# Kernel tuning notes

Hardware: AMD Instinct MI355X
Metric: run time of the kernel (lower is better)

Reference implementation:

```python
import jax, jax.numpy as jnp
import numpy as np

B, L = 64, 8192
WIN = 3            # unfold window size
H = 90             # surrogate MLP hidden width (brains-py default)
N_ELEC = 7         # total electrodes; data on 2,3,4; controls on 0,1,5,6
AMP = 28.5         # electrode_effects amplification


def setup_inputs() -> dict:
    key = jax.random.key(0)
    ks = jax.random.split(key, 16)
    x = jax.random.normal(ks[0], (B, L), dtype=jnp.float32)
    # 4 learned control voltages (electrodes 0,1,5,6), plausible voltage range
    cv = jax.random.uniform(ks[1], (4,), dtype=jnp.float32, minval=-1.2, maxval=0.6)
    def lin(k, fan_in, fan_out):
        w = jax.random.normal(k, (fan_in, fan_out), dtype=jnp.float32) * np.sqrt(2.0 / fan_in).astype(np.float32)
        return w
    W1 = lin(ks[2], N_ELEC, H); b1 = jnp.zeros((H,), jnp.float32)
    W2 = lin(ks[3], H, H);      b2 = jnp.zeros((H,), jnp.float32)
    W3 = lin(ks[4], H, H);      b3 = jnp.zeros((H,), jnp.float32)
    W4 = lin(ks[5], H, H);      b4 = jnp.zeros((H,), jnp.float32)
    W5 = lin(ks[6], H, H);      b5 = jnp.zeros((H,), jnp.float32)
    W6 = lin(ks[7], H, 1);      b6 = jnp.zeros((1,), jnp.float32)
    return {"x": x, "cv": cv,
            "W1": W1, "b1": b1, "W2": W2, "b2": b2, "W3": W3, "b3": b3,
            "W4": W4, "b4": b4, "W5": W5, "b5": b5, "W6": W6, "b6": b6}


def reference(x, cv, W1, b1, W2, b2, W3, b3, W4, b4, W5, b5, W6, b6):
    Bq, Lq = x.shape
    n_win = Lq - WIN + 1
    # sliding windows (unfold(1, 3, 1)): [B, n_win, 3]
    idx = jnp.arange(n_win)[:, None] + jnp.arange(WIN)[None, :]
    win = x[:, idx]  # [B, n_win, 3]
    # assemble 7-electrode input: cv[0:2] | data window | cv[2:4]
    cv_lo = jnp.broadcast_to(cv[:2], (Bq, n_win, 2))
    cv_hi = jnp.broadcast_to(cv[2:], (Bq, n_win, 2))
    z = jnp.concatenate([cv_lo, win, cv_hi], axis=-1)  # [B, n_win, 7]
    h = jax.nn.relu(z @ W1 + b1)
    h = jax.nn.relu(h @ W2 + b2)
    h = jax.nn.relu(h @ W3 + b3)
    h = jax.nn.relu(h @ W4 + b4)
    h = jax.nn.relu(h @ W5 + b5)
    out = (h @ W6 + b6) * AMP  # [B, n_win, 1]
    return out[..., 0]  # squeeze -> [B, n_win]
```

## Files before the change

### kernel.cpp

```cpp
#include <hip/hip_runtime.h>

#define NB   64
#define LSEQ 8192
#define NW   8190
#define HD   90
#define AMPF 28.5f
#define NTILE 2

typedef _Float16 half8  __attribute__((ext_vector_type(8)));
typedef float    f32x16 __attribute__((ext_vector_type(16)));
typedef __fp16   fp16x2 __attribute__((ext_vector_type(2)));

union FragU { uint4 u; half8 h; };

__device__ __forceinline__ unsigned pk2(float a, float b) {
  fp16x2 v = __builtin_amdgcn_cvt_pkrtz(a, b);
  return __builtin_bit_cast(unsigned, v);
}
__device__ __forceinline__ unsigned pkmax0(unsigned w) {
  unsigned r;
  asm("v_pk_max_f16 %0, %1, %2" : "=v"(r) : "v"(w), "v"(0u));
  return r;
}

__global__ void dnpu_pack(const float* __restrict__ W1, const float* __restrict__ b1,
                          const float* __restrict__ W2, const float* __restrict__ b2,
                          const float* __restrict__ W3, const float* __restrict__ b3,
                          const float* __restrict__ W4, const float* __restrict__ b4,
                          const float* __restrict__ W5, const float* __restrict__ b5,
                          const float* __restrict__ W6, const float* __restrict__ b6,
                          uint4* __restrict__ frags) {
  int tid = blockIdx.x * blockDim.x + threadIdx.x;
  if (tid >= 81 * 64) return;
  int f = tid >> 6, lane = tid & 63;
  int n = lane & 31, g = lane >> 5;
  const float* W; const float* bias; int t2, ks, kin, nout;
  if (f < 3) {
    W = W1; bias = b1; t2 = f; ks = 0; kin = 7; nout = HD;
  } else if (f < 75) {
    int q = f - 3; int L = q / 18; int r = q % 18;
    t2 = r / 6; ks = r % 6; kin = HD; nout = HD;
    W    = (L == 0) ? W2 : (L == 1) ? W3 : (L == 2) ? W4 : W5;
    bias = (L == 0) ? b2 : (L == 1) ? b3 : (L == 2) ? b4 : b5;
  } else {
    W = W6; bias = b6; t2 = 0; ks = f - 75; kin = HD; nout = 1;
  }
  int row = 32 * t2 + n;
  FragU u;
#pragma unroll
  for (int i = 0; i < 8; ++i) {
    int k = 16 * ks + 8 * g + i;
    float val = 0.f;
    if (row < nout) {
      if (k < kin)       val = W[k * nout + row];
      else if (k == kin) val = bias[row];
    }
    if (row == HD && k == kin && f < 75) val = 1.0f;
    u.h[i] = (_Float16)val;
  }
  frags[f * 64 + lane] = u.u;
}

__device__ __forceinline__ void trans_u(const f32x16& a, uint4& b0, uint4& b1) {
  unsigned p00 = pkmax0(pk2(a[0],  a[1]));
  unsigned p10 = pkmax0(pk2(a[2],  a[3]));
  unsigned p01 = pkmax0(pk2(a[4],  a[5]));
  unsigned p11 = pkmax0(pk2(a[6],  a[7]));
  unsigned p02 = pkmax0(pk2(a[8],  a[9]));
  unsigned p12 = pkmax0(pk2(a[10], a[11]));
  unsigned p03 = pkmax0(pk2(a[12], a[13]));
  unsigned p13 = pkmax0(pk2(a[14], a[15]));
  asm("v_permlane32_swap_b32 %0, %1" : "+v"(p00), "+v"(p01));
  asm("v_permlane32_swap_b32 %0, %1" : "+v"(p10), "+v"(p11));
  b0 = make_uint4(p00, p10, p01, p11);
  asm("v_permlane32_swap_b32 %0, %1" : "+v"(p02), "+v"(p03));
  asm("v_permlane32_swap_b32 %0, %1" : "+v"(p12), "+v"(p13));
  b1 = make_uint4(p02, p12, p03, p13);
}

__device__ __forceinline__ void hidden_layer_t(const uint4* __restrict__ src, int lane,
                                               uint4 (&B)[6]) {
  uint4 Bn[6];
#pragma unroll
  for (int u = 0; u < 3; ++u) {
    f32x16 a = (f32x16)(0.f);
#pragma unroll
    for (int ks = 0; ks < 6; ++ks) {
      FragU Af; Af.u = src[(u * 6 + ks) * 64 + lane];
      a = __builtin_amdgcn_mfma_f32_32x32x16_f16(
            Af.h, __builtin_bit_cast(half8, B[ks]), a, 0, 0, 0);
    }
    trans_u(a, Bn[2 * u], Bn[2 * u + 1]);
  }
#pragma unroll
  for (int i = 0; i < 6; ++i) B[i] = Bn[i];
}

__global__ __launch_bounds__(512, 2)
void dnpu_mfma(const float* __restrict__ x, const float* __restrict__ cv,
               const uint4* __restrict__ frags, float* __restrict__ out) {
  __shared__ uint4 lfr[72 * 64];
  const int tid  = threadIdx.x;
  const int lane = tid & 63, wid = tid >> 6;
  const int g = lane >> 5, c = lane & 31;
  const int b = blockIdx.y;

  for (int i = tid; i < 72 * 64; i += 512) lfr[i] = frags[3 * 64 + i];
  __syncthreads();

  const float c0 = cv[0], c1 = cv[1], c2 = cv[2], c3 = cv[3];
  const float* xr = x + (size_t)b * LSEQ;
  const int rowbase0 = blockIdx.x * (NTILE * 32 * 8) + wid * (NTILE * 32);

  uint4 Bw[NTILE][6];

#pragma unroll
  for (int t = 0; t < NTILE; ++t) {
    const int w  = rowbase0 + t * 32 + c;
    const int xi = (w < LSEQ - 3) ? w : (LSEQ - 3);
    const float x0 = xr[xi], x1 = xr[xi + 1], x2 = xr[xi + 2];
    half8 B1;
#pragma unroll
    for (int i = 0; i < 8; ++i) B1[i] = (_Float16)0.f;
    if (g == 0) {
      B1[0] = (_Float16)c0; B1[1] = (_Float16)c1;
      B1[2] = (_Float16)x0; B1[3] = (_Float16)x1; B1[4] = (_Float16)x2;
      B1[5] = (_Float16)c2; B1[6] = (_Float16)c3; B1[7] = (_Float16)1.0f;
    }
#pragma unroll
    for (int t2 = 0; t2 < 3; ++t2) {
      FragU Af; Af.u = frags[t2 * 64 + lane];
      f32x16 a = __builtin_amdgcn_mfma_f32_32x32x16_f16(Af.h, B1, (f32x16)(0.f), 0, 0, 0);
      trans_u(a, Bw[t][2 * t2], Bw[t][2 * t2 + 1]);
    }
  }

#pragma unroll
  for (int t = 0; t < NTILE; ++t) hidden_layer_t(&lfr[0 * 18 * 64], lane, Bw[t]);
#pragma unroll
  for (int t = 0; t < NTILE; ++t) hidden_layer_t(&lfr[1 * 18 * 64], lane, Bw[t]);
#pragma unroll
  for (int t = 0; t < NTILE; ++t) hidden_layer_t(&lfr[2 * 18 * 64], lane, Bw[t]);
#pragma unroll
  for (int t = 0; t < NTILE; ++t) hidden_layer_t(&lfr[3 * 18 * 64], lane, Bw[t]);

#pragma unroll
  for (int t = 0; t < NTILE; ++t) {
    f32x16 a = (f32x16)(0.f);
#pragma unroll
    for (int ks = 0; ks < 6; ++ks) {
      FragU Af; Af.u = frags[(75 + ks) * 64 + lane];
      a = __builtin_amdgcn_mfma_f32_32x32x16_f16(
            Af.h, __builtin_bit_cast(half8, Bw[t][ks]), a, 0, 0, 0);
    }
    if (g == 0) {
      const int row = rowbase0 + t * 32 + c;
      if (row < NW) out[(size_t)b * NW + row] = a[0] * AMPF;
    }
  }
}

extern "C" void kernel_launch(void* const* d_in, const int* in_sizes, int n_in,
                              void* d_out, int out_size, void* d_ws, size_t ws_size,
                              hipStream_t stream) {
  const float* x  = (const float*)d_in[0];
  const float* cv = (const float*)d_in[1];
  const float* W1 = (const float*)d_in[2];
  const float* b1 = (const float*)d_in[3];
  const float* W2 = (const float*)d_in[4];
  const float* b2 = (const float*)d_in[5];
  const float* W3 = (const float*)d_in[6];
  const float* b3 = (const float*)d_in[7];
  const float* W4 = (const float*)d_in[8];
  const float* b4 = (const float*)d_in[9];
  const float* W5 = (const float*)d_in[10];
  const float* b5 = (const float*)d_in[11];
  const float* W6 = (const float*)d_in[12];
  const float* b6 = (const float*)d_in[13];
  float* out = (float*)d_out;
  uint4* frags = (uint4*)d_ws;

  hipLaunchKernelGGL(dnpu_pack, dim3(21), dim3(256), 0, stream,
                     W1, b1, W2, b2, W3, b3, W4, b4, W5, b5, W6, b6, frags);
  hipLaunchKernelGGL(dnpu_mfma, dim3(16, NB), dim3(512), 0, stream,
                     x, cv, frags, out);
}
```

Baseline: 46.60 us.

## Interleave four row tiles per wave to reuse weight fragments across MFMAs

Each wave now processes four 32-row tiles instead of two. Every weight fragment loaded from LDS feeds the MFMAs of all tiles before the next fragment is loaded, and four independent accumulator chains are interleaved. The last-layer fragments are hoisted out of the tile loop, and the grid is halved so total coverage stays the same. The intent is to cut LDS traffic and hide MFMA dependency latency, at the cost of many more live VGPRs (four 16-float accumulators plus 24 uint4 B fragments), which under launch_bounds(512,2) may cause spills, and of fewer workgroups.

```diff
diff --git a/kernel.cpp b/kernel.cpp
--- a/kernel.cpp
+++ b/kernel.cpp
@@ -5,7 +5,7 @@
 #define NW   8190
 #define HD   90
 #define AMPF 28.5f
-#define NTILE 2
+#define NTILE 4
 
 typedef _Float16 half8  __attribute__((ext_vector_type(8)));
 typedef float    f32x16 __attribute__((ext_vector_type(16)));
@@ -78,22 +78,29 @@
   b1 = make_uint4(p02, p12, p03, p13);
 }
 
-__device__ __forceinline__ void hidden_layer_t(const uint4* __restrict__ src, int lane,
-                                               uint4 (&B)[6]) {
-  uint4 Bn[6];
+__device__ __forceinline__ void hidden_layer(const uint4* __restrict__ src, int lane,
+                                             uint4 (&Bw)[NTILE][6]) {
+  uint4 Bn[NTILE][6];
 #pragma unroll
   for (int u = 0; u < 3; ++u) {
-    f32x16 a = (f32x16)(0.f);
+    f32x16 a[NTILE];
+#pragma unroll
+    for (int t = 0; t < NTILE; ++t) a[t] = (f32x16)(0.f);
 #pragma unroll
     for (int ks = 0; ks < 6; ++ks) {
       FragU Af; Af.u = src[(u * 6 + ks) * 64 + lane];
-      a = __builtin_amdgcn_mfma_f32_32x32x16_f16(
-            Af.h, __builtin_bit_cast(half8, B[ks]), a, 0, 0, 0);
+#pragma unroll
+      for (int t = 0; t < NTILE; ++t)
+        a[t] = __builtin_amdgcn_mfma_f32_32x32x16_f16(
+                 Af.h, __builtin_bit_cast(half8, Bw[t][ks]), a[t], 0, 0, 0);
     }
-    trans_u(a, Bn[2 * u], Bn[2 * u + 1]);
+#pragma unroll
+    for (int t = 0; t < NTILE; ++t) trans_u(a[t], Bn[t][2 * u], Bn[t][2 * u + 1]);
   }
 #pragma unroll
-  for (int i = 0; i < 6; ++i) B[i] = Bn[i];
+  for (int t = 0; t < NTILE; ++t)
+#pragma unroll
+    for (int i = 0; i < 6; ++i) Bw[t][i] = Bn[t][i];
 }
 
 __global__ __launch_bounds__(512, 2)
@@ -135,27 +142,26 @@
     }
   }
 
+  hidden_layer(&lfr[0 * 18 * 64], lane, Bw);
+  hidden_layer(&lfr[1 * 18 * 64], lane, Bw);
+  hidden_layer(&lfr[2 * 18 * 64], lane, Bw);
+  hidden_layer(&lfr[3 * 18 * 64], lane, Bw);
+
+  {
+    FragU Af6[6];
 #pragma unroll
-  for (int t = 0; t < NTILE; ++t) hidden_layer_t(&lfr[0 * 18 * 64], lane, Bw[t]);
+    for (int ks = 0; ks < 6; ++ks) Af6[ks].u = frags[(75 + ks) * 64 + lane];
 #pragma unroll
-  for (int t = 0; t < NTILE; ++t) hidden_layer_t(&lfr[1 * 18 * 64], lane, Bw[t]);
+    for (int t = 0; t < NTILE; ++t) {
+      f32x16 a = (f32x16)(0.f);
 #pragma unroll
-  for (int t = 0; t < NTILE; ++t) hidden_layer_t(&lfr[2 * 18 * 64], lane, Bw[t]);
-#pragma unroll
-  for (int t = 0; t < NTILE; ++t) hidden_layer_t(&lfr[3 * 18 * 64], lane, Bw[t]);
-
-#pragma unroll
-  for (int t = 0; t < NTILE; ++t) {
-    f32x16 a = (f32x16)(0.f);
-#pragma unroll
-    for (int ks = 0; ks < 6; ++ks) {
-      FragU Af; Af.u = frags[(75 + ks) * 64 + lane];
-      a = __builtin_amdgcn_mfma_f32_32x32x16_f16(
-            Af.h, __builtin_bit_cast(half8, Bw[t][ks]), a, 0, 0, 0);
-    }
-    if (g == 0) {
-      const int row = rowbase0 + t * 32 + c;
-      if (row < NW) out[(size_t)b * NW + row] = a[0] * AMPF;
+      for (int ks = 0; ks < 6; ++ks)
+        a = __builtin_amdgcn_mfma_f32_32x32x16_f16(
+              Af6[ks].h, __builtin_bit_cast(half8, Bw[t][ks]), a, 0, 0, 0);
+      if (g == 0) {
+        const int row = rowbase0 + t * 32 + c;
+        if (row < NW) out[(size_t)b * NW + row] = a[0] * AMPF;
+      }
     }
   }
 }
@@ -182,6 +188,6 @@
 
   hipLaunchKernelGGL(dnpu_pack, dim3(21), dim3(256), 0, stream,
                      W1, b1, W2, b2, W3, b3, W4, b4, W5, b5, W6, b6, frags);
-  hipLaunchKernelGGL(dnpu_mfma, dim3(16, NB), dim3(512), 0, stream,
+  hipLaunchKernelGGL(dnpu_mfma, dim3(8, NB), dim3(512), 0, stream,
                      x, cv, frags, out);
 }
```

Result: faster. 44.47 us (-4.6%).

## Interleave two tiles' MFMA clusters and double-buffer layer weights in LDS

Applied to the files above, without the earlier changes.

Splits each hidden layer into output-chunk clusters and interleaves the two row tiles, so one tile's MFMA chain runs while the other's results are converted and transposed. LDS weight storage shrinks from four layers to a two-layer double buffer that is refilled between layers, which adds block-wide barriers. Blocks shrink to 256 threads and the grid doubles, and the final-layer weight fragments are loaded once and reused for both tiles. The extra barriers and LDS refill traffic could offset the gains from better latency hiding and lower LDS use.

```diff
diff --git a/kernel.cpp b/kernel.cpp
--- a/kernel.cpp
+++ b/kernel.cpp
@@ -5,7 +5,6 @@
 #define NW   8190
 #define HD   90
 #define AMPF 28.5f
-#define NTILE 2
 
 typedef _Float16 half8  __attribute__((ext_vector_type(8)));
 typedef float    f32x16 __attribute__((ext_vector_type(16)));
@@ -78,44 +77,58 @@
   b1 = make_uint4(p02, p12, p03, p13);
 }
 
-__device__ __forceinline__ void hidden_layer_t(const uint4* __restrict__ src, int lane,
-                                               uint4 (&B)[6]) {
-  uint4 Bn[6];
-#pragma unroll
-  for (int u = 0; u < 3; ++u) {
-    f32x16 a = (f32x16)(0.f);
-#pragma unroll
-    for (int ks = 0; ks < 6; ++ks) {
-      FragU Af; Af.u = src[(u * 6 + ks) * 64 + lane];
-      a = __builtin_amdgcn_mfma_f32_32x32x16_f16(
-            Af.h, __builtin_bit_cast(half8, B[ks]), a, 0, 0, 0);
-    }
-    trans_u(a, Bn[2 * u], Bn[2 * u + 1]);
-  }
-#pragma unroll
-  for (int i = 0; i < 6; ++i) B[i] = Bn[i];
-}
-
-__global__ __launch_bounds__(512, 2)
+__device__ __forceinline__ f32x16 cluster(const uint4* __restrict__ src, int u, int lane,
+                                          const uint4 (&B)[6]) {
+  f32x16 a = (f32x16)(0.f);
+#pragma unroll
+  for (int ks = 0; ks < 6; ++ks) {
+    FragU Af; Af.u = src[(u * 6 + ks) * 64 + lane];
+    a = __builtin_amdgcn_mfma_f32_32x32x16_f16(
+          Af.h, __builtin_bit_cast(half8, B[ks]), a, 0, 0, 0);
+  }
+  return a;
+}
+
+__device__ __forceinline__ void layer_pipe(const uint4* __restrict__ src, int lane,
+                                           const uint4 (&B0)[6], const uint4 (&B1)[6],
+                                           uint4 (&O0)[6], uint4 (&O1)[6]) {
+  f32x16 a00 = cluster(src, 0, lane, B0);
+  f32x16 a10 = cluster(src, 0, lane, B1);
+  f32x16 a01 = cluster(src, 1, lane, B0);
+  trans_u(a00, O0[0], O0[1]);
+  f32x16 a11 = cluster(src, 1, lane, B1);
+  trans_u(a10, O1[0], O1[1]);
+  f32x16 a02 = cluster(src, 2, lane, B0);
+  trans_u(a01, O0[2], O0[3]);
+  f32x16 a12 = cluster(src, 2, lane, B1);
+  trans_u(a11, O1[2], O1[3]);
+  trans_u(a02, O0[4], O0[5]);
+  trans_u(a12, O1[4], O1[5]);
+}
+
+__global__ __launch_bounds__(256, 2)
 void dnpu_mfma(const float* __restrict__ x, const float* __restrict__ cv,
                const uint4* __restrict__ frags, float* __restrict__ out) {
-  __shared__ uint4 lfr[72 * 64];
+  __shared__ uint4 lfr[2][18 * 64];
   const int tid  = threadIdx.x;
   const int lane = tid & 63, wid = tid >> 6;
   const int g = lane >> 5, c = lane & 31;
   const int b = blockIdx.y;
 
-  for (int i = tid; i < 72 * 64; i += 512) lfr[i] = frags[3 * 64 + i];
+  for (int i = tid; i < 18 * 64; i += 256) {
+    lfr[0][i] = frags[3 * 64 + i];
+    lfr[1][i] = frags[21 * 64 + i];
+  }
   __syncthreads();
 
   const float c0 = cv[0], c1 = cv[1], c2 = cv[2], c3 = cv[3];
   const float* xr = x + (size_t)b * LSEQ;
-  const int rowbase0 = blockIdx.x * (NTILE * 32 * 8) + wid * (NTILE * 32);
-
-  uint4 Bw[NTILE][6];
-
-#pragma unroll
-  for (int t = 0; t < NTILE; ++t) {
+  const int rowbase0 = blockIdx.x * 256 + wid * 64;
+
+  uint4 Bw[2][6], Bv[2][6];
+
+#pragma unroll
+  for (int t = 0; t < 2; ++t) {
     const int w  = rowbase0 + t * 32 + c;
     const int xi = (w < LSEQ - 3) ? w : (LSEQ - 3);
     const float x0 = xr[xi], x1 = xr[xi + 1], x2 = xr[xi + 2];
@@ -135,27 +148,32 @@
     }
   }
 
-#pragma unroll
-  for (int t = 0; t < NTILE; ++t) hidden_layer_t(&lfr[0 * 18 * 64], lane, Bw[t]);
-#pragma unroll
-  for (int t = 0; t < NTILE; ++t) hidden_layer_t(&lfr[1 * 18 * 64], lane, Bw[t]);
-#pragma unroll
-  for (int t = 0; t < NTILE; ++t) hidden_layer_t(&lfr[2 * 18 * 64], lane, Bw[t]);
-#pragma unroll
-  for (int t = 0; t < NTILE; ++t) hidden_layer_t(&lfr[3 * 18 * 64], lane, Bw[t]);
-
-#pragma unroll
-  for (int t = 0; t < NTILE; ++t) {
-    f32x16 a = (f32x16)(0.f);
-#pragma unroll
-    for (int ks = 0; ks < 6; ++ks) {
-      FragU Af; Af.u = frags[(75 + ks) * 64 + lane];
-      a = __builtin_amdgcn_mfma_f32_32x32x16_f16(
-            Af.h, __builtin_bit_cast(half8, Bw[t][ks]), a, 0, 0, 0);
-    }
-    if (g == 0) {
-      const int row = rowbase0 + t * 32 + c;
-      if (row < NW) out[(size_t)b * NW + row] = a[0] * AMPF;
+  layer_pipe(&lfr[0][0], lane, Bw[0], Bw[1], Bv[0], Bv[1]);
+  __syncthreads();
+  for (int i = tid; i < 18 * 64; i += 256) lfr[0][i] = frags[39 * 64 + i];
+  __syncthreads();
+  layer_pipe(&lfr[1][0], lane, Bv[0], Bv[1], Bw[0], Bw[1]);
+  __syncthreads();
+  for (int i = tid; i < 18 * 64; i += 256) lfr[1][i] = frags[57 * 64 + i];
+  __syncthreads();
+  layer_pipe(&lfr[0][0], lane, Bw[0], Bw[1], Bv[0], Bv[1]);
+  layer_pipe(&lfr[1][0], lane, Bv[0], Bv[1], Bw[0], Bw[1]);
+
+  {
+    FragU Af6[6];
+#pragma unroll
+    for (int ks = 0; ks < 6; ++ks) Af6[ks].u = frags[(75 + ks) * 64 + lane];
+#pragma unroll
+    for (int t = 0; t < 2; ++t) {
+      f32x16 a = (f32x16)(0.f);
+#pragma unroll
+      for (int ks = 0; ks < 6; ++ks)
+        a = __builtin_amdgcn_mfma_f32_32x32x16_f16(
+              Af6[ks].h, __builtin_bit_cast(half8, Bw[t][ks]), a, 0, 0, 0);
+      if (g == 0) {
+        const int row = rowbase0 + t * 32 + c;
+        if (row < NW) out[(size_t)b * NW + row] = a[0] * AMPF;
+      }
     }
   }
 }
@@ -182,6 +200,6 @@
 
   hipLaunchKernelGGL(dnpu_pack, dim3(21), dim3(256), 0, stream,
                      W1, b1, W2, b2, W3, b3, W4, b4, W5, b5, W6, b6, frags);
-  hipLaunchKernelGGL(dnpu_mfma, dim3(16, NB), dim3(512), 0, stream,
+  hipLaunchKernelGGL(dnpu_mfma, dim3(32, NB), dim3(256), 0, stream,
                      x, cv, frags, out);
 }
```

Measured after the change: 45.64 us. 1.02x faster.
